# Kernel optimization log

Measured on AMD Instinct MI355X. Metric: run time of the kernel, lower is better.

## Reference

```python
import jax, jax.numpy as jnp
import numpy as np

N = 50000
E = 800000
IN_C = 128
HID = 32
HEADS = 4
OUT_C = 128
NEG_SLOPE = 0.2


def setup_inputs() -> dict:
    key = jax.random.key(0)
    ks = jax.random.split(key, 12)
    x = jax.random.normal(ks[0], (N, IN_C), dtype=jnp.float32)
    edge_index = jax.random.randint(ks[1], (2, E), 0, N, dtype=jnp.int32)
    s1 = 1.0 / np.sqrt(IN_C)
    s2 = 1.0 / np.sqrt(HEADS * HID)
    return {
        "x": x,
        "edge_index": edge_index,
        # conv1: in_channels -> hidden*heads, concat=True
        "W1l": jax.random.normal(ks[2], (IN_C, HEADS * HID), dtype=jnp.float32) * s1,
        "W1r": jax.random.normal(ks[3], (IN_C, HEADS * HID), dtype=jnp.float32) * s1,
        "att1": jax.random.normal(ks[4], (HEADS, HID), dtype=jnp.float32) * (1.0 / np.sqrt(HID)),
        "b1": jnp.zeros((HEADS * HID,), dtype=jnp.float32),
        # conv2: hidden*heads -> out_channels, heads=1, concat=False
        "W2l": jax.random.normal(ks[5], (HEADS * HID, OUT_C), dtype=jnp.float32) * s2,
        "W2r": jax.random.normal(ks[6], (HEADS * HID, OUT_C), dtype=jnp.float32) * s2,
        "att2": jax.random.normal(ks[7], (1, OUT_C), dtype=jnp.float32) * (1.0 / np.sqrt(OUT_C)),
        "b2": jnp.zeros((OUT_C,), dtype=jnp.float32),
    }


def gatv2_conv(x, src, dst, Wl, Wr, att, bias, heads, out_per_head, concat):
    n = x.shape[0]
    xl = (x @ Wl).reshape(n, heads, out_per_head)   # source transform [N,H,C]
    xr = (x @ Wr).reshape(n, heads, out_per_head)   # target transform [N,H,C]
    m = xl[src] + xr[dst]                           # [E,H,C]
    e = jnp.sum(jax.nn.leaky_relu(m, NEG_SLOPE) * att, axis=-1)  # [E,H]
    # segment softmax over incoming edges of each destination node
    mx = jax.ops.segment_max(e, dst, num_segments=n)             # [N,H]
    ex = jnp.exp(e - mx[dst])                                    # [E,H]
    denom = jax.ops.segment_sum(ex, dst, num_segments=n)         # [N,H]
    alpha = ex / jnp.where(denom[dst] == 0, 1.0, denom[dst])     # [E,H]
    out = jax.ops.segment_sum(alpha[:, :, None] * xl[src], dst, num_segments=n)  # [N,H,C]
    if concat:
        out = out.reshape(n, heads * out_per_head)
    else:
        out = out.mean(axis=1)
    return out + bias


def reference(x, edge_index, W1l, W1r, att1, b1, W2l, W2r, att2, b2):
    src, dst = edge_index[0], edge_index[1]
    h = gatv2_conv(x, src, dst, W1l, W1r, att1, b1, HEADS, HID, concat=True)
    h = jax.nn.elu(h)
    out = gatv2_conv(h, src, dst, W2l, W2r, att2, b2, 1, OUT_C, concat=False)
    return out
```

## Files before the change

### kernel.cpp

```cpp
#include <hip/hip_runtime.h>
#include <math.h>

#define IN_C 128
#define NEG_SLOPE 0.2f
#define LOG2E 1.44269504f

typedef unsigned int uint_t;
typedef unsigned short ushort_t;
typedef _Float16 half8_t __attribute__((ext_vector_type(8)));
typedef _Float16 half2_t __attribute__((ext_vector_type(2)));
typedef float floatx4 __attribute__((ext_vector_type(4)));

__device__ __forceinline__ float fdot2f(half2_t a, half2_t b, float c) {
#if __has_builtin(__builtin_amdgcn_fdot2)
    return __builtin_amdgcn_fdot2(a, b, c, false);
#else
    return fmaf((float)a[1], (float)b[1], fmaf((float)a[0], (float)b[0], c));
#endif
}
#define H2(v, i) ((half2_t){(v)[2 * (i)], (v)[2 * (i) + 1]})

__device__ __forceinline__ float fexp2(float x) {
#if __has_builtin(__builtin_amdgcn_exp2f)
    return __builtin_amdgcn_exp2f(x);
#else
    return exp2f(x);
#endif
}

template <int CTRL>
__device__ __forceinline__ float dpp_addf(float x) {
    int y = __builtin_amdgcn_update_dpp(0, __float_as_int(x), CTRL, 0xF, 0xF, true);
    return x + __int_as_float(y);
}

#define XPAD 136
template <bool IN_HALF>
__global__ __launch_bounds__(256) void transform_mfma(
        const void* __restrict__ xin,
        const float* __restrict__ Wl,
        const float* __restrict__ Wr,
        _Float16* __restrict__ outl,
        _Float16* __restrict__ outr, int n) {
    __shared__ _Float16 xs[16 * XPAD + 8];
    const int tid  = threadIdx.x;
    const int wv   = tid >> 6;
    const int l    = tid & 63;
    const int lm   = l & 15;
    const int quad = l >> 4;
    const int kb   = quad * 8;

    const float* Wsel = (wv < 2) ? Wl : Wr;
    _Float16*    osel = (wv < 2) ? outl : outr;
    const int nbase = (wv & 1) * 64;
    half8_t bw[4][4];
#pragma unroll
    for (int t = 0; t < 4; ++t) {
        const int ncol = nbase + t * 16 + lm;
#pragma unroll
        for (int K = 0; K < 4; ++K) {
            const int k0 = K * 32 + kb;
            half8_t h;
#pragma unroll
            for (int j = 0; j < 8; ++j)
                h[j] = (_Float16)Wsel[(size_t)(k0 + j) * IN_C + ncol];
            bw[t][K] = h;
        }
    }

    const int nStrips = (n + 15) >> 4;
    for (int s = blockIdx.x; s < nStrips; s += gridDim.x) {
        const int row0 = s * 16;
        __syncthreads();
        {
            const int srow = tid >> 4;
            const int scol = (tid & 15) * 8;
            const int grow = row0 + srow;
            half8_t h;
#pragma unroll
            for (int j = 0; j < 8; ++j) h[j] = (_Float16)0.f;
            if (grow < n) {
                if constexpr (IN_HALF) {
                    h = *(const half8_t*)&((const _Float16*)xin)[(size_t)grow * IN_C + scol];
                } else {
                    const float4 v0 = *(const float4*)&((const float*)xin)[(size_t)grow * IN_C + scol];
                    const float4 v1 = *(const float4*)&((const float*)xin)[(size_t)grow * IN_C + scol + 4];
                    h[0] = (_Float16)v0.x; h[1] = (_Float16)v0.y;
                    h[2] = (_Float16)v0.z; h[3] = (_Float16)v0.w;
                    h[4] = (_Float16)v1.x; h[5] = (_Float16)v1.y;
                    h[6] = (_Float16)v1.z; h[7] = (_Float16)v1.w;
                }
            }
            *(half8_t*)&xs[srow * XPAD + scol] = h;
        }
        __syncthreads();
        half8_t af[4];
#pragma unroll
        for (int K = 0; K < 4; ++K)
            af[K] = *(half8_t*)&xs[lm * XPAD + K * 32 + kb];
        floatx4 acc[4];
#pragma unroll
        for (int t = 0; t < 4; ++t) acc[t] = (floatx4){0.f, 0.f, 0.f, 0.f};
#pragma unroll
        for (int t = 0; t < 4; ++t)
#pragma unroll
            for (int K = 0; K < 4; ++K)
                acc[t] = __builtin_amdgcn_mfma_f32_16x16x32_f16(af[K], bw[t][K], acc[t], 0, 0, 0);
#pragma unroll
        for (int t = 0; t < 4; ++t) {
            const int col = nbase + t * 16 + lm;
#pragma unroll
            for (int r = 0; r < 4; ++r) {
                const int row = row0 + quad * 4 + r;
                if (row < n) osel[(size_t)row * IN_C + col] = (_Float16)acc[t][r];
            }
        }
    }
}

__global__ void hist_kernel(const int* __restrict__ dst, int* __restrict__ cnt,
                            ushort_t* __restrict__ rank, int E) {
    int e = blockIdx.x * blockDim.x + threadIdx.x;
    if (e < E) {
        int r = atomicAdd(&cnt[dst[e]], 1);
        rank[e] = (ushort_t)r;
    }
}

__global__ void scan_block_sums(const int* __restrict__ cnt, int* __restrict__ part, int n) {
    __shared__ int sdata[256];
    int t = threadIdx.x;
    int i = blockIdx.x * 256 + t;
    sdata[t] = (i < n) ? ((cnt[i] + 3) & ~3) : 0;
    __syncthreads();
    for (int o = 128; o >= 1; o >>= 1) {
        if (t < o) sdata[t] += sdata[t + o];
        __syncthreads();
    }
    if (t == 0) part[blockIdx.x] = sdata[0];
}

__global__ void scan_part_excl(int* __restrict__ part, int nb) {
    __shared__ int buf[1024];
    int t = threadIdx.x;
    int v = (t < nb) ? part[t] : 0;
    buf[t] = v;
    __syncthreads();
    for (int o = 1; o < 1024; o <<= 1) {
        int a = (t >= o) ? buf[t - o] : 0;
        __syncthreads();
        buf[t] += a;
        __syncthreads();
    }
    if (t < nb) part[t] = buf[t] - v;
}

__global__ void scan_final(const int* __restrict__ cnt, const int* __restrict__ part,
                           int* __restrict__ rowptr, int n) {
    __shared__ int buf[256];
    int t = threadIdx.x;
    int i = blockIdx.x * 256 + t;
    int v = (i < n) ? ((cnt[i] + 3) & ~3) : 0;
    buf[t] = v;
    __syncthreads();
    for (int o = 1; o < 256; o <<= 1) {
        int a = (t >= o) ? buf[t - o] : 0;
        __syncthreads();
        buf[t] += a;
        __syncthreads();
    }
    int excl = part[blockIdx.x] + buf[t] - v;
    if (i < n) rowptr[i] = excl;
    if (i == n - 1) rowptr[n] = excl + v;
}

__global__ void scatter_csr(const int* __restrict__ src,
                            const int* __restrict__ dst,
                            const int* __restrict__ rowptr,
                            const ushort_t* __restrict__ rank,
                            ushort_t* __restrict__ gsrc, int E) {
    int e = blockIdx.x * blockDim.x + threadIdx.x;
    if (e >= E) return;
    int pos = rowptr[dst[e]] + (int)rank[e];
    gsrc[pos] = (ushort_t)src[e];
}

template <int LAYER>
__global__ __launch_bounds__(256) void node_fused(
        const _Float16* __restrict__ xlb,
        const _Float16* __restrict__ xr,
        const float* __restrict__ att,
        const int* __restrict__ rowptr,
        const int* __restrict__ cnt,
        const ushort_t* __restrict__ gsrc,
        const float* __restrict__ bias,
        void* __restrict__ outp, int N) {
    const int l = threadIdx.x & 63;
    const int q = l & 15;
    const int d = blockIdx.x * 16 + (threadIdx.x >> 4);
    if (d >= N) return;
    const int beg = rowptr[d];
    const int deg = cnt[d];
    const int nt  = (deg + 3) >> 2;
    const int cb  = q * 8;

    const half8_t xrv = *(const half8_t*)&xr[(size_t)d * IN_C + cb];
    const float4 A0 = *(const float4*)&att[cb];
    const float4 A1 = *(const float4*)&att[cb + 4];
    const float afv[8] = {A0.x, A0.y, A0.z, A0.w, A1.x, A1.y, A1.z, A1.w};
    half8_t a6, a4;
#pragma unroll
    for (int j = 0; j < 8; ++j) {
        a6[j] = (_Float16)(0.6f * LOG2E * afv[j]);
        a4[j] = (_Float16)(0.4f * LOG2E * afv[j]);
    }

    float m = -1e30f, ls = 0.f;
    float acc[8] = {0.f, 0.f, 0.f, 0.f, 0.f, 0.f, 0.f, 0.f};

    const uint2* gp = (const uint2*)(gsrc + beg);
    half8_t xc[4];
    uint2 g1;
    if (nt > 0) {
        uint2 g0 = gp[0];
        g1 = gp[(1 < nt) ? 1 : 0];
        uint_t i0 = g0.x & 0xffffu, i1 = g0.x >> 16;
        uint_t i2 = g0.y & 0xffffu, i3 = g0.y >> 16;
        xc[0] = *(const half8_t*)(xlb + (i0 << 7) + cb);
        xc[1] = *(const half8_t*)(xlb + (i1 << 7) + cb);
        xc[2] = *(const half8_t*)(xlb + (i2 << 7) + cb);
        xc[3] = *(const half8_t*)(xlb + (i3 << 7) + cb);
    }

    for (int t = 0; t < nt; ++t) {
        const int t2 = (t + 2 < nt) ? t + 2 : nt - 1;
        uint2 g2 = gp[t2];
        half8_t xn[4];
        {
            uint_t i0 = g1.x & 0xffffu, i1 = g1.x >> 16;
            uint_t i2 = g1.y & 0xffffu, i3 = g1.y >> 16;
            xn[0] = *(const half8_t*)(xlb + (i0 << 7) + cb);
            xn[1] = *(const half8_t*)(xlb + (i1 << 7) + cb);
            xn[2] = *(const half8_t*)(xlb + (i2 << 7) + cb);
            xn[3] = *(const half8_t*)(xlb + (i3 << 7) + cb);
        }
        float f[4];
#pragma unroll
        for (int u = 0; u < 4; ++u) {
            half8_t tv = xc[u] + xrv;
            uint4 tu = __builtin_bit_cast(uint4, tv);
            tu.x &= 0x7fff7fffu; tu.y &= 0x7fff7fffu;
            tu.z &= 0x7fff7fffu; tu.w &= 0x7fff7fffu;
            half8_t av = __builtin_bit_cast(half8_t, tu);
            float p = 0.f;
#pragma unroll
            for (int j = 0; j < 4; ++j) p = fdot2f(H2(tv, j), H2(a6, j), p);
#pragma unroll
            for (int j = 0; j < 4; ++j) p = fdot2f(H2(av, j), H2(a4, j), p);
            p = dpp_addf<0xB1>(p);
            p = dpp_addf<0x4E>(p);
            if (LAYER == 2) {
                p = dpp_addf<0x141>(p);
                p = dpp_addf<0x140>(p);
            }
            f[u] = (4 * t + u < deg) ? p : -1e30f;
        }
        float bm = fmaxf(fmaxf(f[0], f[1]), fmaxf(f[2], f[3]));
        if (!__all(bm <= m + 5.7708f)) {
            float nm = fmaxf(m, bm);
            float fc = fexp2(m - nm);
            ls *= fc;
#pragma unroll
            for (int j = 0; j < 8; ++j) acc[j] *= fc;
            m = nm;
        }
#pragma unroll
        for (int u = 0; u < 4; ++u) {
            float wgt = fexp2(f[u] - m);
            ls += wgt;
#pragma unroll
            for (int j = 0; j < 8; ++j)
                acc[j] = fmaf((float)xc[u][j], wgt, acc[j]);
        }
#pragma unroll
        for (int u = 0; u < 4; ++u) xc[u] = xn[u];
        g1 = g2;
    }

    const float inv = (ls > 0.f) ? 1.f / ls : 0.f;
    const float4 b0 = *(const float4*)&bias[cb];
    const float4 b1 = *(const float4*)&bias[cb + 4];
    const float bf[8] = {b0.x, b0.y, b0.z, b0.w, b1.x, b1.y, b1.z, b1.w};
    if (LAYER == 1) {
        half8_t h;
#pragma unroll
        for (int j = 0; j < 8; ++j) {
            float o = acc[j] * inv + bf[j];
            o = (o > 0.f) ? o : fexp2(o * LOG2E) - 1.f;
            h[j] = (_Float16)o;
        }
        *(half8_t*)&((_Float16*)outp)[(size_t)d * IN_C + cb] = h;
    } else {
        float4 o1, o2;
        o1.x = acc[0] * inv + bf[0]; o1.y = acc[1] * inv + bf[1];
        o1.z = acc[2] * inv + bf[2]; o1.w = acc[3] * inv + bf[3];
        o2.x = acc[4] * inv + bf[4]; o2.y = acc[5] * inv + bf[5];
        o2.z = acc[6] * inv + bf[6]; o2.w = acc[7] * inv + bf[7];
        *(float4*)&((float*)outp)[(size_t)d * IN_C + cb]     = o1;
        *(float4*)&((float*)outp)[(size_t)d * IN_C + cb + 4] = o2;
    }
}

extern "C" void kernel_launch(void* const* d_in, const int* in_sizes, int n_in,
                              void* d_out, int out_size, void* d_ws, size_t ws_size,
                              hipStream_t stream) {
    const float* x    = (const float*)d_in[0];
    const int*   ei   = (const int*)d_in[1];
    const float* W1l  = (const float*)d_in[2];
    const float* W1r  = (const float*)d_in[3];
    const float* att1 = (const float*)d_in[4];
    const float* b1   = (const float*)d_in[5];
    const float* W2l  = (const float*)d_in[6];
    const float* W2r  = (const float*)d_in[7];
    const float* att2 = (const float*)d_in[8];
    const float* b2   = (const float*)d_in[9];

    const int N = in_sizes[0] / IN_C;
    const int E = in_sizes[1] / 2;
    const int* src = ei;
    const int* dst = ei + E;

    float* ws = (float*)d_ws;
    size_t o = 0;
    _Float16* xlh = (_Float16*)(ws + o); o += (size_t)N * IN_C / 2;
    _Float16* xrh = (_Float16*)(ws + o); o += (size_t)N * IN_C / 2;
    _Float16* hb  = (_Float16*)(ws + o); o += (size_t)N * IN_C / 2;
    int* iws    = (int*)(ws + o);
    int* rowptr = iws;
    int* cnt    = rowptr + (N + 1);
    int* part   = cnt + N;
    ushort_t* rank = (ushort_t*)(part + 1024);
    ushort_t* gsrc = rank + ((size_t)E + 64);
    const size_t gsrc_bytes = ((size_t)E + 4 * (size_t)N + 64) * sizeof(ushort_t);

    hipMemsetAsync(cnt, 0, (size_t)N * 4, stream);
    hipMemsetAsync(gsrc, 0, gsrc_bytes, stream);

    const int B = 256;
    const int nb = (N + 255) / 256;
    hist_kernel<<<(E + B - 1) / B, B, 0, stream>>>(dst, cnt, rank, E);
    scan_block_sums<<<nb, 256, 0, stream>>>(cnt, part, N);
    scan_part_excl<<<1, 1024, 0, stream>>>(part, nb);
    scan_final<<<nb, 256, 0, stream>>>(cnt, part, rowptr, N);
    scatter_csr<<<(E + B - 1) / B, B, 0, stream>>>(src, dst, rowptr, rank, gsrc, E);

    transform_mfma<false><<<512, 256, 0, stream>>>(x, W1l, W1r, xlh, xrh, N);
    node_fused<1><<<(N + 15) / 16, 256, 0, stream>>>(xlh, xrh, att1, rowptr, cnt, gsrc, b1, hb, N);

    transform_mfma<true><<<512, 256, 0, stream>>>(hb, W2l, W2r, xlh, xrh, N);
    node_fused<2><<<(N + 15) / 16, 256, 0, stream>>>(xlh, xrh, att2, rowptr, cnt, gsrc, b2, d_out, N);
}
```

Measured before the change: 253.0 us.

## Deepen gather prefetch to three tiles and zero only CSR padding slots

The node aggregation loop now keeps two tiles of gathered source features in flight instead of one, which hides more of the random-gather latency at the cost of extra registers. The full memset of the padded neighbor index array is removed. Instead, scan_final zeroes only the few padding slots per node beyond its degree. This drops a separate fill pass over the index buffer.

```diff
diff --git a/kernel.cpp b/kernel.cpp
--- a/kernel.cpp
+++ b/kernel.cpp
@@ -156,11 +156,12 @@
 }
 
 __global__ void scan_final(const int* __restrict__ cnt, const int* __restrict__ part,
-                           int* __restrict__ rowptr, int n) {
+                           int* __restrict__ rowptr, ushort_t* __restrict__ gsrc, int n) {
     __shared__ int buf[256];
     int t = threadIdx.x;
     int i = blockIdx.x * 256 + t;
-    int v = (i < n) ? ((cnt[i] + 3) & ~3) : 0;
+    int deg = (i < n) ? cnt[i] : 0;
+    int v = (deg + 3) & ~3;
     buf[t] = v;
     __syncthreads();
     for (int o = 1; o < 256; o <<= 1) {
@@ -170,7 +171,10 @@
         __syncthreads();
     }
     int excl = part[blockIdx.x] + buf[t] - v;
-    if (i < n) rowptr[i] = excl;
+    if (i < n) {
+        rowptr[i] = excl;
+        for (int p = excl + deg; p < excl + v; ++p) gsrc[p] = 0;
+    }
     if (i == n - 1) rowptr[n] = excl + v;
 }
 
@@ -219,30 +223,37 @@
     float acc[8] = {0.f, 0.f, 0.f, 0.f, 0.f, 0.f, 0.f, 0.f};
 
     const uint2* gp = (const uint2*)(gsrc + beg);
-    half8_t xc[4];
-    uint2 g1;
+    half8_t xc[4], xn[4];
+    uint2 g2;
     if (nt > 0) {
         uint2 g0 = gp[0];
-        g1 = gp[(1 < nt) ? 1 : 0];
+        uint2 g1 = gp[(1 < nt) ? 1 : 0];
+        g2 = gp[(2 < nt) ? 2 : nt - 1];
         uint_t i0 = g0.x & 0xffffu, i1 = g0.x >> 16;
         uint_t i2 = g0.y & 0xffffu, i3 = g0.y >> 16;
         xc[0] = *(const half8_t*)(xlb + (i0 << 7) + cb);
         xc[1] = *(const half8_t*)(xlb + (i1 << 7) + cb);
         xc[2] = *(const half8_t*)(xlb + (i2 << 7) + cb);
         xc[3] = *(const half8_t*)(xlb + (i3 << 7) + cb);
+        i0 = g1.x & 0xffffu; i1 = g1.x >> 16;
+        i2 = g1.y & 0xffffu; i3 = g1.y >> 16;
+        xn[0] = *(const half8_t*)(xlb + (i0 << 7) + cb);
+        xn[1] = *(const half8_t*)(xlb + (i1 << 7) + cb);
+        xn[2] = *(const half8_t*)(xlb + (i2 << 7) + cb);
+        xn[3] = *(const half8_t*)(xlb + (i3 << 7) + cb);
     }
 
     for (int t = 0; t < nt; ++t) {
-        const int t2 = (t + 2 < nt) ? t + 2 : nt - 1;
-        uint2 g2 = gp[t2];
-        half8_t xn[4];
+        const int t3 = (t + 3 < nt) ? t + 3 : nt - 1;
+        uint2 g3 = gp[t3];
+        half8_t x2[4];
         {
-            uint_t i0 = g1.x & 0xffffu, i1 = g1.x >> 16;
-            uint_t i2 = g1.y & 0xffffu, i3 = g1.y >> 16;
-            xn[0] = *(const half8_t*)(xlb + (i0 << 7) + cb);
-            xn[1] = *(const half8_t*)(xlb + (i1 << 7) + cb);
-            xn[2] = *(const half8_t*)(xlb + (i2 << 7) + cb);
-            xn[3] = *(const half8_t*)(xlb + (i3 << 7) + cb);
+            uint_t i0 = g2.x & 0xffffu, i1 = g2.x >> 16;
+            uint_t i2 = g2.y & 0xffffu, i3 = g2.y >> 16;
+            x2[0] = *(const half8_t*)(xlb + (i0 << 7) + cb);
+            x2[1] = *(const half8_t*)(xlb + (i1 << 7) + cb);
+            x2[2] = *(const half8_t*)(xlb + (i2 << 7) + cb);
+            x2[3] = *(const half8_t*)(xlb + (i3 << 7) + cb);
         }
         float f[4];
 #pragma unroll
@@ -283,8 +294,8 @@
                 acc[j] = fmaf((float)xc[u][j], wgt, acc[j]);
         }
 #pragma unroll
-        for (int u = 0; u < 4; ++u) xc[u] = xn[u];
-        g1 = g2;
+        for (int u = 0; u < 4; ++u) { xc[u] = xn[u]; xn[u] = x2[u]; }
+        g2 = g3;
     }
 
     const float inv = (ls > 0.f) ? 1.f / ls : 0.f;
@@ -341,17 +352,16 @@
     int* part   = cnt + N;
     ushort_t* rank = (ushort_t*)(part + 1024);
     ushort_t* gsrc = rank + ((size_t)E + 64);
-    const size_t gsrc_bytes = ((size_t)E + 4 * (size_t)N + 64) * sizeof(ushort_t);
+    (void)ws_size;
 
     hipMemsetAsync(cnt, 0, (size_t)N * 4, stream);
-    hipMemsetAsync(gsrc, 0, gsrc_bytes, stream);
 
     const int B = 256;
     const int nb = (N + 255) / 256;
     hist_kernel<<<(E + B - 1) / B, B, 0, stream>>>(dst, cnt, rank, E);
     scan_block_sums<<<nb, 256, 0, stream>>>(cnt, part, N);
     scan_part_excl<<<1, 1024, 0, stream>>>(part, nb);
-    scan_final<<<nb, 256, 0, stream>>>(cnt, part, rowptr, N);
+    scan_final<<<nb, 256, 0, stream>>>(cnt, part, rowptr, gsrc, N);
     scatter_csr<<<(E + B - 1) / B, B, 0, stream>>>(src, dst, rowptr, rank, gsrc, E);
 
     transform_mfma<false><<<512, 256, 0, stream>>>(x, W1l, W1r, xlh, xrh, N);
```

After: 247.2 us (median of 2 runs). 2.3% less time.
